# Kernel tuning notes

Measured on AMD Instinct MI355X. Metric: run time of the kernel, lower is better.

Reference implementation:

```python
import jax, jax.numpy as jnp
import numpy as np

B, T, C, H, L, V = 8, 512, 512, 8, 2, 512
DH = C // H
SCALE = 1.0 / np.sqrt(DH)


def _ln(x, g, b):
    mu = jnp.mean(x, -1, keepdims=True)
    var = jnp.mean((x - mu) ** 2, -1, keepdims=True)
    return (x - mu) * jax.lax.rsqrt(var + 1e-5) * g + b


def setup_inputs() -> dict:
    key = jax.random.key(0)
    ks = jax.random.split(key, 16)
    f = lambda k, shape: jax.random.normal(k, shape, jnp.float32) * 0.02
    return {
        "idx": jax.random.randint(ks[0], (B, T), 0, 4),
        "tok_emb": f(ks[1], (4, C)),
        "pos_emb": f(ks[2], (T, C)),
        "ln1_g": jnp.ones((L, C)), "ln1_b": jnp.zeros((L, C)),
        "Wq": f(ks[3], (L, C, C)), "bq": jnp.zeros((L, C)),
        "Wk": f(ks[4], (L, C, C)), "bk": jnp.zeros((L, C)),
        "Wv": f(ks[5], (L, C, C)), "bv": jnp.zeros((L, C)),
        "Wp": f(ks[6], (L, C, C)), "bp": jnp.zeros((L, C)),
        "ln2_g": jnp.ones((L, C)), "ln2_b": jnp.zeros((L, C)),
        "W1": f(ks[7], (L, C, 4 * C)), "b1": jnp.zeros((L, 4 * C)),
        "W2": f(ks[8], (L, 4 * C, C)), "b2": jnp.zeros((L, C)),
        "lnf_g": jnp.ones((C,)), "lnf_b": jnp.zeros((C,)),
        "Whead": f(ks[9], (C, V)),
        "steps": 4,
    }


def _block(x, p):
    (l1g, l1b, wq, bq, wk, bk, wv, bv, wp, bp,
     l2g, l2b, w1, b1, w2, b2) = p
    # attention (mask buffer is all ones in the original -> full attention)
    xn = _ln(x, l1g, l1b)
    q = (xn @ wq + bq).reshape(B, T, H, DH)
    k = (xn @ wk + bk).reshape(B, T, H, DH)
    v = (xn @ wv + bv).reshape(B, T, H, DH)
    att = jnp.einsum('bqhd,bkhd->bhqk', q, k) * SCALE
    att = jax.nn.softmax(att, axis=-1)
    y = jnp.einsum('bhqk,bkhd->bqhd', att, v).reshape(B, T, C)
    x = x + y @ wp + bp
    # MLP with exact (erf) GELU, matching torch nn.GELU default
    h = jax.nn.gelu(_ln(x, l2g, l2b) @ w1 + b1, approximate=False)
    return x + h @ w2 + b2


def reference(idx, tok_emb, pos_emb, ln1_g, ln1_b, Wq, bq, Wk, bk, Wv, bv,
              Wp, bp, ln2_g, ln2_b, W1, b1, W2, b2, lnf_g, lnf_b, Whead,
              steps):
    params = (ln1_g, ln1_b, Wq, bq, Wk, bk, Wv, bv, Wp, bp,
              ln2_g, ln2_b, W1, b1, W2, b2)
    x = tok_emb[idx] + pos_emb[None, :, :]

    def run_blocks(x):
        def step(x, p):
            return _block(x, p), None
        x, _ = jax.lax.scan(step, x, params)
        return x

    for _ in range(steps):  # recurrent application of the whole stack
        x = run_blocks(x)
    x = _ln(x, lnf_g, lnf_b)
    return x @ Whead  # logits [B, T, V]
```

## Files before the change

kernel.cpp:

```cpp
#include <hip/hip_runtime.h>
#include <hip/hip_bf16.h>
#include <math.h>

#define BB 8
#define TT 512
#define CC 512
#define HH 8
#define DH 64
#define LL 2
#define VV 512
#define NSTEPS 4
#define BT (BB*TT)
#define FF (4*CC)

typedef unsigned short u16;
typedef __bf16 bf16x8 __attribute__((ext_vector_type(8)));
typedef float f32x4 __attribute__((ext_vector_type(4)));
typedef u16 u16x8 __attribute__((ext_vector_type(8)));

static __device__ __forceinline__ u16 f2bf(float f) {
    unsigned int u = __float_as_uint(f);
    unsigned int r = (u + 0x7fffu + ((u >> 16) & 1u)) >> 16;
    return (u16)r;
}

static __device__ __forceinline__ void async16(const void* g, void* l) {
    __builtin_amdgcn_global_load_lds((__attribute__((address_space(1))) void*)g,
                                     (__attribute__((address_space(3))) void*)l, 16, 0, 0);
}

static __device__ __forceinline__ int swzp(int r) { return (r ^ (r >> 2)) & 7; }

__global__ __launch_bounds__(256)
void prologue_kernel(const float* __restrict__ Wq, const float* __restrict__ Wk,
                     const float* __restrict__ Wv, const float* __restrict__ Wp,
                     const float* __restrict__ W1, const float* __restrict__ W2,
                     const float* __restrict__ Wh,
                     const float* __restrict__ ln1g, const float* __restrict__ ln1b,
                     const float* __restrict__ ln2g, const float* __restrict__ ln2b,
                     const float* __restrict__ lnfg, const float* __restrict__ lnfb,
                     u16* w_qkvt, u16* w_pt, u16* w_1t, u16* w_2t, u16* w_ht,
                     const int* __restrict__ idx, const float* __restrict__ tok,
                     const float* __restrict__ pos, float* __restrict__ x,
                     u16* __restrict__ xb, float* __restrict__ ucb,
                     float2* __restrict__ sp) {
    int bid = blockIdx.x;
    const size_t wcc = (size_t)CC*CC, wcf = (size_t)CC*FF;
    if (bid >= 1630) {
        int bt = bid - 1630;
        int t  = threadIdx.x;
        int token = idx[bt];
        int posrow = bt & (TT - 1);
        float v0 = tok[token*CC + t]       + pos[posrow*CC + t];
        float v1 = tok[token*CC + t + 256] + pos[posrow*CC + t + 256];
        size_t base = (size_t)bt*CC;
        x[base + t] = v0;            x[base + t + 256] = v1;
        xb[base + t] = f2bf(v0);     xb[base + t + 256] = f2bf(v1);
        float s = v0 + v1, q = v0*v0 + v1*v1;
#pragma unroll
        for (int off = 1; off < 64; off <<= 1) { s += __shfl_xor(s, off); q += __shfl_xor(q, off); }
        __shared__ float rs[4], rq[4];
        int wid = t >> 6, lane = t & 63;
        if (lane == 0) { rs[wid] = s; rq[wid] = q; }
        __syncthreads();
        if (t == 0)      sp[(size_t)bt*8] = make_float2(rs[0]+rs[1]+rs[2]+rs[3],
                                                        rq[0]+rq[1]+rq[2]+rq[3]);
        else if (t < 8)  sp[(size_t)bt*8 + t] = make_float2(0.f, 0.f);
        return;
    }
    if (bid >= 1600) {
        int c = (bid - 1600)*256 + threadIdx.x;
        const float* Wsrc; const float* gv; const float* bv2; float* up; float* cp;
        int n, Nd;
        if (c < 3072) {
            int l = c / 1536, w = c % 1536, m = w / 512; n = w % 512; Nd = CC;
            Wsrc = (m == 0 ? Wq : (m == 1 ? Wk : Wv)) + l*wcc;
            gv = ln1g + l*CC; bv2 = ln1b + l*CC;
            up = ucb + c; cp = ucb + 3072 + c;
        } else if (c < 7168) {
            int d = c - 3072, l = d / 2048; n = d % 2048; Nd = FF;
            Wsrc = W1 + l*wcf; gv = ln2g + l*CC; bv2 = ln2b + l*CC;
            up = ucb + 6144 + d; cp = ucb + 10240 + d;
        } else {
            n = c - 7168; Nd = VV; Wsrc = Wh; gv = lnfg; bv2 = lnfb;
            up = ucb + 14336 + n; cp = ucb + 14848 + n;
        }
        float su = 0.f, sc = 0.f;
        for (int k = 0; k < CC; k++) {
            float w = Wsrc[(size_t)k*Nd + n];
            su += gv[k]*w; sc += bv2[k]*w;
        }
        *up = su; *cp = sc;
        return;
    }
    const float* src; u16* dst; const float* gv = nullptr; int K, N, i0, j0;
    if (bid < 1536) {
        int l = bid / 768, r = bid % 768;
        if (r < 256) {
            int m = r / 64, t = r % 64;
            K = CC; N = CC;
            i0 = (t / 8) * 64; j0 = (t % 8) * 64;
            if      (m == 0) { src = Wq + l*wcc; dst = w_qkvt + (size_t)l*3*wcc;          gv = ln1g + l*CC; }
            else if (m == 1) { src = Wk + l*wcc; dst = w_qkvt + (size_t)l*3*wcc + wcc;    gv = ln1g + l*CC; }
            else if (m == 2) { src = Wv + l*wcc; dst = w_qkvt + (size_t)l*3*wcc + 2*wcc;  gv = ln1g + l*CC; }
            else             { src = Wp + l*wcc; dst = w_pt + (size_t)l*wcc; }
        } else if (r < 512) {
            int t = r - 256;
            K = CC; N = FF;
            i0 = (t / 32) * 64; j0 = (t % 32) * 64;
            src = W1 + l*wcf; dst = w_1t + (size_t)l*wcf; gv = ln2g + l*CC;
        } else {
            int t = r - 512;
            K = FF; N = CC;
            i0 = (t / 8) * 64; j0 = (t % 8) * 64;
            src = W2 + l*wcf; dst = w_2t + (size_t)l*wcf;
        }
    } else {
        int t = bid - 1536;
        K = CC; N = CC;
        i0 = (t / 8) * 64; j0 = (t % 8) * 64;
        src = Wh; dst = w_ht; gv = lnfg;
    }
    __shared__ float tile[64][65];
    int tt = threadIdx.x;
    int rr = tt >> 2, cg = (tt & 3) * 16;
    float gk = gv ? gv[i0 + rr] : 1.0f;
#pragma unroll
    for (int i = 0; i < 16; i++)
        tile[rr][cg + i] = src[(size_t)(i0 + rr) * N + j0 + cg + i] * gk;
    __syncthreads();
#pragma unroll
    for (int i = 0; i < 16; i++)
        dst[(size_t)(j0 + rr) * K + i0 + cg + i] = f2bf(tile[cg + i][rr]);
}

template<int BM, int BN, int THREADS, int WROWS, int WCOLS, int EPI>
__global__ __launch_bounds__(THREADS, 6)
void gemm_bt_kernel(const u16* __restrict__ A, const u16* __restrict__ Bt,
                    int N, int K,
                    const float* __restrict__ bias, const float* __restrict__ biask,
                    const float* __restrict__ biasv,
                    const float* __restrict__ uvec, const float* __restrict__ cvec,
                    const float2* __restrict__ spin, float2* __restrict__ spout,
                    float* outf, u16* outq, u16* outk, u16* outvt) {
    constexpr int WTM = BM / WROWS, WTN = BN / WCOLS;
    constexpr int TM = WTM / 16, TN = WTN / 16;
    constexpr bool FOLD = (EPI == 0 || EPI == 2 || EPI == 3);
    static_assert(THREADS == WROWS * WCOLS * 64, "wave grid");
    static_assert((8*BM) % THREADS == 0 && (8*BN) % THREADS == 0, "staging divisibility");
    static_assert(EPI != 1 || (BM == 32 && BN == 64 && WROWS == 2 && WCOLS == 2), "stats layout");
    __shared__ u16 lds_a[2][2][BM][32];
    __shared__ u16 lds_b[2][2][BN][32];
    __shared__ float s_rs[FOLD ? BM : 1], s_mrs[FOLD ? BM : 1];
    __shared__ float psum[EPI == 1 ? 2 : 1][BM], psq[EPI == 1 ? 2 : 1][BM];
    int tid = threadIdx.x;
    int wid = tid >> 6, lane = tid & 63;
    int quad = lane >> 4, l15 = lane & 15;
    int wm = (wid % WROWS) * WTM, wn = (wid / WROWS) * WTN;

    int NBN = N / BN;
    int lin = blockIdx.x;
    int x8 = lin & 7, slot = lin >> 3;
    int bn = slot % NBN;
    int bm = (slot / NBN) * 8 + x8;

    const size_t a0 = (size_t)bm * BM, b0 = (size_t)bn * BN;

    auto stage = [&](int buf, int kt) {
#pragma unroll
        for (int i = 0; i < (8*BM)/THREADS; i++) {
            int f = tid + i*THREADS;
            int ks2 = f / (4*BM), rem = f % (4*BM);
            int row = rem >> 2, c2 = rem & 3;
            int g = (ks2*4 + c2) ^ swzp(row);
            async16(&A[(a0 + row)*K + kt + g*8], (u16*)lds_a[buf] + (size_t)f*8);
        }
#pragma unroll
        for (int i = 0; i < (8*BN)/THREADS; i++) {
            int f = tid + i*THREADS;
            int ks2 = f / (4*BN), rem = f % (4*BN);
            int row = rem >> 2, c2 = rem & 3;
            int g = (ks2*4 + c2) ^ swzp(row);
            async16(&Bt[(b0 + row)*K + kt + g*8], (u16*)lds_b[buf] + (size_t)f*8);
        }
    };

    f32x4 zero = {0.f, 0.f, 0.f, 0.f};
    f32x4 acc[TM][TN];
#pragma unroll
    for (int mi = 0; mi < TM; mi++)
#pragma unroll
        for (int ni = 0; ni < TN; ni++) acc[mi][ni] = zero;

    stage(0, 0);
    __syncthreads();
    const int NKT = K / 64;
    for (int kt = 0; kt < NKT; kt++) {
        int cur = kt & 1;
        if (kt + 1 < NKT) stage(cur ^ 1, (kt + 1) * 64);
#pragma unroll
        for (int ks = 0; ks < 2; ks++) {
            bf16x8 af[TM], bfr[TN];
#pragma unroll
            for (int mi = 0; mi < TM; mi++) {
                int row = wm + mi*16 + l15;
                int lc = (ks*4 + quad) ^ swzp(row);
                af[mi] = *(const bf16x8*)&lds_a[cur][lc >> 2][row][(lc & 3) * 8];
            }
#pragma unroll
            for (int ni = 0; ni < TN; ni++) {
                int row = wn + ni*16 + l15;
                int lc = (ks*4 + quad) ^ swzp(row);
                bfr[ni] = *(const bf16x8*)&lds_b[cur][lc >> 2][row][(lc & 3) * 8];
            }
#pragma unroll
            for (int mi = 0; mi < TM; mi++)
#pragma unroll
                for (int ni = 0; ni < TN; ni++)
                    acc[mi][ni] = __builtin_amdgcn_mfma_f32_16x16x32_bf16(af[mi], bfr[ni], acc[mi][ni], 0, 0, 0);
        }
        __syncthreads();
    }

    if (FOLD) {
        for (int r = tid; r < BM; r += THREADS) {
            float s = 0.f, q = 0.f;
#pragma unroll
            for (int j = 0; j < 8; j++) { float2 p = spin[(a0 + r)*8 + j]; s += p.x; q += p.y; }
            float mu  = s * (1.0f / CC);
            float var = q * (1.0f / CC) - mu * mu;
            float rstd = rsqrtf(var + 1e-5f);
            s_rs[r] = rstd; s_mrs[r] = mu * rstd;
        }
        __syncthreads();
    }

    float lsum[TM][4], lsq[TM][4];
    if (EPI == 1) {
#pragma unroll
        for (int mi = 0; mi < TM; mi++)
#pragma unroll
            for (int i = 0; i < 4; i++) { lsum[mi][i] = 0.f; lsq[mi][i] = 0.f; }
    }

#pragma unroll
    for (int mi = 0; mi < TM; mi++)
#pragma unroll
        for (int ni = 0; ni < TN; ni++) {
            int col = bn*BN + wn + ni*16 + l15;
            float uc_ = 0.f, cc_ = 0.f;
            if (FOLD) { uc_ = uvec[col]; cc_ = cvec[col]; }
#pragma unroll
            for (int i = 0; i < 4; i++) {
                int rloc = wm + mi*16 + quad*4 + i;
                int row = bm*BM + rloc;
                float v = acc[mi][ni][i];
                if (FOLD) v = s_rs[rloc]*v - s_mrs[rloc]*uc_ + cc_;
                if (EPI == 0) {
                    int region = col >> 9, cl = col & 511;
                    if (region == 0) {
                        v = (v + bias[cl]) * 0.125f;
                        outq[(size_t)row*512 + cl] = f2bf(v);
                    } else if (region == 1) {
                        v += biask[cl];
                        outk[(size_t)row*512 + cl] = f2bf(v);
                    } else {
                        v += biasv[cl];
                        int bb = row >> 9, tpos = row & 511, hh = cl >> 6, dh = cl & 63;
                        outvt[(((size_t)(bb*8 + hh)*64 + dh) << 9) + tpos] = f2bf(v);
                    }
                } else if (EPI == 1) {
                    size_t id2 = (size_t)row * N + col;
                    v += bias[col] + outf[id2];
                    outf[id2] = v;
                    outq[id2] = f2bf(v);
                    lsum[mi][i] += v; lsq[mi][i] += v*v;
                } else if (EPI == 2) {
                    v += bias[col];
                    v = 0.5f * v * (1.0f + erff(v * 0.70710678118654752f));
                    outq[(size_t)row * N + col] = f2bf(v);
                } else {
                    outf[(size_t)row * N + col] = v;
                }
            }
        }

    if (EPI == 1) {
#pragma unroll
        for (int mi = 0; mi < TM; mi++)
#pragma unroll
            for (int i = 0; i < 4; i++) {
                float s = lsum[mi][i], q = lsq[mi][i];
#pragma unroll
                for (int off = 1; off < 16; off <<= 1) { s += __shfl_xor(s, off); q += __shfl_xor(q, off); }
                if (l15 == 0) {
                    int pr = wm + mi*16 + quad*4 + i;
                    psum[wn >> 5][pr] = s; psq[wn >> 5][pr] = q;
                }
            }
        __syncthreads();
        if (tid < BM) {
            spout[(a0 + tid)*8 + bn] = make_float2(psum[0][tid] + psum[1][tid],
                                                   psq[0][tid] + psq[1][tid]);
        }
    }
}

__global__ __launch_bounds__(256)
void attn_mfma_kernel(const u16* __restrict__ q, const u16* __restrict__ k,
                      const u16* __restrict__ vt, u16* __restrict__ y) {
    __shared__ u16 lq[64][64];
    __shared__ u16 lk[2][64][64];
    __shared__ u16 lv[2][64][64];
    __shared__ u16 lp[4][16][72];
    int qt = blockIdx.x, h = blockIdx.y, b = blockIdx.z;
    int tid = threadIdx.x;
    int wid = tid >> 6, lane = tid & 63;
    int quad = lane >> 4, l15 = lane & 15;
    const int sr = tid >> 3;
    const int sc = (tid & 7) * 8;
    const int gsc = (((tid & 7) ^ swzp(sr)) << 3);

    auto stageKV = [&](int buf, int kt) {
#pragma unroll
        for (int c = 0; c < 2; c++) {
            async16(&k[(size_t)(b*TT + kt*64 + c*32 + sr)*CC + h*DH + gsc], &lk[buf][c*32 + sr][sc]);
            async16(&vt[((size_t)((b*HH + h)*DH + c*32 + sr))*TT + kt*64 + gsc], &lv[buf][c*32 + sr][sc]);
        }
    };

#pragma unroll
    for (int c = 0; c < 2; c++)
        async16(&q[(size_t)(b*TT + qt*64 + c*32 + sr)*CC + h*DH + gsc], &lq[c*32 + sr][sc]);
    stageKV(0, 0);
    __syncthreads();

    f32x4 zero = {0.f, 0.f, 0.f, 0.f};
    f32x4 acc_o[4];
    float m_st[4], l_st[4];
#pragma unroll
    for (int i = 0; i < 4; i++) { m_st[i] = -INFINITY; l_st[i] = 0.f; }
#pragma unroll
    for (int ni = 0; ni < 4; ni++) acc_o[ni] = zero;

    const int rowq = wid*16 + l15;
    const int pq = swzp(rowq);

    for (int kt = 0; kt < TT/64; kt++) {
        int cur = kt & 1;
        if (kt + 1 < TT/64) stageKV(cur ^ 1, kt + 1);

        f32x4 s[4];
#pragma unroll
        for (int ni = 0; ni < 4; ni++) s[ni] = zero;
#pragma unroll
        for (int ks = 0; ks < 2; ks++) {
            int lcq = (ks*4 + quad) ^ pq;
            bf16x8 aq = *(const bf16x8*)&lq[rowq][lcq * 8];
            bf16x8 bfr[4];
#pragma unroll
            for (int ni = 0; ni < 4; ni++) {
                int rowk = ni*16 + l15;
                int lck = (ks*4 + quad) ^ swzp(rowk);
                bfr[ni] = *(const bf16x8*)&lk[cur][rowk][lck * 8];
            }
#pragma unroll
            for (int ni = 0; ni < 4; ni++)
                s[ni] = __builtin_amdgcn_mfma_f32_16x16x32_bf16(aq, bfr[ni], s[ni], 0, 0, 0);
        }

#pragma unroll
        for (int i = 0; i < 4; i++) {
            float mx = -INFINITY;
#pragma unroll
            for (int ni = 0; ni < 4; ni++) mx = fmaxf(mx, s[ni][i]);
#pragma unroll
            for (int off = 1; off < 16; off <<= 1) mx = fmaxf(mx, __shfl_xor(mx, off));
            float mn = fmaxf(m_st[i], mx);
            float al = __expf(m_st[i] - mn);
            float rs = 0.f;
#pragma unroll
            for (int ni = 0; ni < 4; ni++) {
                float p = __expf(s[ni][i] - mn);
                s[ni][i] = p;
                rs += p;
            }
#pragma unroll
            for (int off = 1; off < 16; off <<= 1) rs += __shfl_xor(rs, off);
            l_st[i] = l_st[i] * al + rs;
            m_st[i] = mn;
#pragma unroll
            for (int ni = 0; ni < 4; ni++) acc_o[ni][i] *= al;
        }

#pragma unroll
        for (int ni = 0; ni < 4; ni++)
#pragma unroll
            for (int i = 0; i < 4; i++)
                lp[wid][quad*4 + i][ni*16 + l15] = f2bf(s[ni][i]);

#pragma unroll
        for (int ks = 0; ks < 2; ks++) {
            bf16x8 pa = *(const bf16x8*)&lp[wid][l15][ks*32 + quad*8];
            bf16x8 vb[4];
#pragma unroll
            for (int ni = 0; ni < 4; ni++) {
                int rowv = ni*16 + l15;
                int lcv = (ks*4 + quad) ^ swzp(rowv);
                vb[ni] = *(const bf16x8*)&lv[cur][rowv][lcv * 8];
            }
#pragma unroll
            for (int ni = 0; ni < 4; ni++)
                acc_o[ni] = __builtin_amdgcn_mfma_f32_16x16x32_bf16(pa, vb[ni], acc_o[ni], 0, 0, 0);
        }
        __syncthreads();
    }

#pragma unroll
    for (int i = 0; i < 4; i++) {
        float inv = 1.0f / l_st[i];
#pragma unroll
        for (int ni = 0; ni < 4; ni++) {
            int qrow = qt*64 + wid*16 + quad*4 + i;
            int col  = h*DH + ni*16 + l15;
            y[(size_t)(b*TT + qrow)*CC + col] = f2bf(acc_o[ni][i] * inv);
        }
    }
}

extern "C" void kernel_launch(void* const* d_in, const int* in_sizes, int n_in,
                              void* d_out, int out_size, void* d_ws, size_t ws_size,
                              hipStream_t stream) {
    const int*   idx   = (const int*)d_in[0];
    const float* tok   = (const float*)d_in[1];
    const float* pos   = (const float*)d_in[2];
    const float* ln1g  = (const float*)d_in[3];
    const float* ln1b  = (const float*)d_in[4];
    const float* Wq    = (const float*)d_in[5];
    const float* bq    = (const float*)d_in[6];
    const float* Wk    = (const float*)d_in[7];
    const float* bk    = (const float*)d_in[8];
    const float* Wv    = (const float*)d_in[9];
    const float* bv    = (const float*)d_in[10];
    const float* Wp    = (const float*)d_in[11];
    const float* bp    = (const float*)d_in[12];
    const float* ln2g  = (const float*)d_in[13];
    const float* ln2b  = (const float*)d_in[14];
    const float* W1    = (const float*)d_in[15];
    const float* b1    = (const float*)d_in[16];
    const float* W2    = (const float*)d_in[17];
    const float* b2    = (const float*)d_in[18];
    const float* lnfg  = (const float*)d_in[19];
    const float* lnfb  = (const float*)d_in[20];
    const float* Whead = (const float*)d_in[21];

    float* x  = (float*)d_ws;
    u16* xb   = (u16*)(x + (size_t)BT*CC);
    u16* yb   = xb + (size_t)BT*CC;
    u16* R    = yb + (size_t)BT*CC;
    u16* qb   = R;
    u16* kb   = R + (size_t)BT*CC;
    u16* vtb  = R + (size_t)2*BT*CC;
    u16* hb   = R;
    u16* w_qkvt = R + (size_t)4*BT*CC;
    u16* w_pt   = w_qkvt + (size_t)2*3*CC*CC;
    u16* w_1t   = w_pt   + (size_t)2*CC*CC;
    u16* w_2t   = w_1t   + (size_t)2*CC*FF;
    u16* w_ht   = w_2t   + (size_t)2*FF*CC;
    float* ucb  = (float*)(w_ht + (size_t)CC*VV);
    float2* sp  = (float2*)(ucb + 15360);

    prologue_kernel<<<1630 + BT, 256, 0, stream>>>(Wq, Wk, Wv, Wp, W1, W2, Whead,
                                                   ln1g, ln1b, ln2g, ln2b, lnfg, lnfb,
                                                   w_qkvt, w_pt, w_1t, w_2t, w_ht,
                                                   idx, tok, pos, x, xb, ucb, sp);

    const int g_qkv  = (3*CC/128) * (BT/64);
    const int g_fc1  = (FF/128)   * (BT/64);
    const int g_pf   = (CC/64)    * (BT/32);
    const int g_head = (VV/64)    * (BT/32);

    for (int s = 0; s < NSTEPS; s++) {
        for (int l = 0; l < LL; l++) {
            gemm_bt_kernel<64,128,512,2,4,0><<<g_qkv, 512, 0, stream>>>(
                xb, w_qkvt + (size_t)l*3*CC*CC, 3*CC, CC,
                bq + l*CC, bk + l*CC, bv + l*CC,
                ucb + l*1536, ucb + 3072 + l*1536, sp, nullptr,
                nullptr, qb, kb, vtb);
            attn_mfma_kernel<<<dim3(TT/64, HH, BB), 256, 0, stream>>>(qb, kb, vtb, yb);
            gemm_bt_kernel<32,64,256,2,2,1><<<g_pf, 256, 0, stream>>>(
                yb, w_pt + (size_t)l*CC*CC, CC, CC,
                bp + l*CC, nullptr, nullptr,
                nullptr, nullptr, nullptr, sp,
                x, xb, nullptr, nullptr);
            gemm_bt_kernel<64,128,512,2,4,2><<<g_fc1, 512, 0, stream>>>(
                xb, w_1t + (size_t)l*CC*FF, FF, CC,
                b1 + (size_t)l*FF, nullptr, nullptr,
                ucb + 6144 + l*2048, ucb + 10240 + l*2048, sp, nullptr,
                nullptr, hb, nullptr, nullptr);
            gemm_bt_kernel<32,64,256,2,2,1><<<g_pf, 256, 0, stream>>>(
                hb, w_2t + (size_t)l*FF*CC, CC, FF,
                b2 + l*CC, nullptr, nullptr,
                nullptr, nullptr, nullptr, sp,
                x, xb, nullptr, nullptr);
        }
    }

    gemm_bt_kernel<32,64,256,2,2,3><<<g_head, 256, 0, stream>>>(
        xb, w_ht, VV, CC,
        nullptr, nullptr, nullptr,
        ucb + 14336, ucb + 14848, sp, nullptr,
        (float*)d_out, nullptr, nullptr, nullptr);
}
```

Baseline: 907.6 us.

## Split LN-fold reductions over K, vectorize prologue, transpose attention score MFMA

The prologue's per-column LayerNorm-fold dot products are split across 8 K-chunks written to partial buffers, which the GEMM epilogues sum at read time. This gives more parallel blocks in place of a serial 512-long loop. The embedding and weight-transpose paths now use vector loads and stores, and the embedding path handles two rows per block. The attention kernel swaps the QK^T MFMA operands so each lane holds one query row, cutting softmax shuffles to two steps and enabling vectorized P stores to LDS. The cost is 8 extra loads per column in every fold epilogue and a cross-lane shuffle to broadcast alpha and l.

```diff
diff --git a/kernel.cpp b/kernel.cpp
--- a/kernel.cpp
+++ b/kernel.cpp
@@ -17,6 +17,7 @@
 typedef __bf16 bf16x8 __attribute__((ext_vector_type(8)));
 typedef float f32x4 __attribute__((ext_vector_type(4)));
 typedef u16 u16x8 __attribute__((ext_vector_type(8)));
+typedef u16 u16x4 __attribute__((ext_vector_type(4)));
 
 static __device__ __forceinline__ u16 f2bf(float f) {
     unsigned int u = __float_as_uint(f);
@@ -46,51 +47,64 @@
                      float2* __restrict__ sp) {
     int bid = blockIdx.x;
     const size_t wcc = (size_t)CC*CC, wcf = (size_t)CC*FF;
-    if (bid >= 1630) {
-        int bt = bid - 1630;
+    if (bid >= 1840) {
+        int eb = bid - 1840;
         int t  = threadIdx.x;
-        int token = idx[bt];
-        int posrow = bt & (TT - 1);
-        float v0 = tok[token*CC + t]       + pos[posrow*CC + t];
-        float v1 = tok[token*CC + t + 256] + pos[posrow*CC + t + 256];
-        size_t base = (size_t)bt*CC;
-        x[base + t] = v0;            x[base + t + 256] = v1;
-        xb[base + t] = f2bf(v0);     xb[base + t + 256] = f2bf(v1);
-        float s = v0 + v1, q = v0*v0 + v1*v1;
+        int r  = t >> 7, c4 = t & 127;
+        int row = eb*2 + r;
+        int token = idx[row];
+        int posrow = row & (TT - 1);
+        f32x4 v = ((const f32x4*)(tok + (size_t)token*CC))[c4]
+                + ((const f32x4*)(pos + (size_t)posrow*CC))[c4];
+        size_t base = (size_t)row*CC;
+        ((f32x4*)(x + base))[c4] = v;
+        u16x4 o;
+#pragma unroll
+        for (int j = 0; j < 4; j++) o[j] = f2bf(v[j]);
+        *(u16x4*)&xb[base + c4*4] = o;
+        float s = v[0]+v[1]+v[2]+v[3];
+        float q = v[0]*v[0]+v[1]*v[1]+v[2]*v[2]+v[3]*v[3];
 #pragma unroll
         for (int off = 1; off < 64; off <<= 1) { s += __shfl_xor(s, off); q += __shfl_xor(q, off); }
         __shared__ float rs[4], rq[4];
         int wid = t >> 6, lane = t & 63;
         if (lane == 0) { rs[wid] = s; rq[wid] = q; }
         __syncthreads();
-        if (t == 0)      sp[(size_t)bt*8] = make_float2(rs[0]+rs[1]+rs[2]+rs[3],
-                                                        rq[0]+rq[1]+rq[2]+rq[3]);
-        else if (t < 8)  sp[(size_t)bt*8 + t] = make_float2(0.f, 0.f);
+        if (t < 16) {
+            int r2 = t >> 3, slot = t & 7;
+            float2 val = (slot == 0)
+                ? make_float2(rs[r2*2] + rs[r2*2+1], rq[r2*2] + rq[r2*2+1])
+                : make_float2(0.f, 0.f);
+            sp[(size_t)(eb*2 + r2)*8 + slot] = val;
+        }
         return;
     }
     if (bid >= 1600) {
-        int c = (bid - 1600)*256 + threadIdx.x;
-        const float* Wsrc; const float* gv; const float* bv2; float* up; float* cp;
+        int d  = bid - 1600;
+        int j  = d & 7;
+        int cb = d >> 3;
+        int c  = cb*256 + threadIdx.x;
+        const float* Wsrc; const float* gv; const float* bv2;
         int n, Nd;
         if (c < 3072) {
             int l = c / 1536, w = c % 1536, m = w / 512; n = w % 512; Nd = CC;
             Wsrc = (m == 0 ? Wq : (m == 1 ? Wk : Wv)) + l*wcc;
             gv = ln1g + l*CC; bv2 = ln1b + l*CC;
-            up = ucb + c; cp = ucb + 3072 + c;
         } else if (c < 7168) {
-            int d = c - 3072, l = d / 2048; n = d % 2048; Nd = FF;
+            int dd = c - 3072, l = dd / 2048; n = dd % 2048; Nd = FF;
             Wsrc = W1 + l*wcf; gv = ln2g + l*CC; bv2 = ln2b + l*CC;
-            up = ucb + 6144 + d; cp = ucb + 10240 + d;
         } else {
             n = c - 7168; Nd = VV; Wsrc = Wh; gv = lnfg; bv2 = lnfb;
-            up = ucb + 14336 + n; cp = ucb + 14848 + n;
         }
         float su = 0.f, sc = 0.f;
-        for (int k = 0; k < CC; k++) {
-            float w = Wsrc[(size_t)k*Nd + n];
-            su += gv[k]*w; sc += bv2[k]*w;
-        }
-        *up = su; *cp = sc;
+        int k0 = j*64;
+#pragma unroll 4
+        for (int kk = 0; kk < 64; kk++) {
+            float w = Wsrc[(size_t)(k0 + kk)*Nd + n];
+            su += gv[k0 + kk]*w; sc += bv2[k0 + kk]*w;
+        }
+        ucb[j*7680 + c]         = su;
+        ucb[61440 + j*7680 + c] = sc;
         return;
     }
     const float* src; u16* dst; const float* gv = nullptr; int K, N, i0, j0;
@@ -122,16 +136,29 @@
         src = Wh; dst = w_ht; gv = lnfg;
     }
     __shared__ float tile[64][65];
+    __shared__ float gl[64];
     int tt = threadIdx.x;
     int rr = tt >> 2, cg = (tt & 3) * 16;
-    float gk = gv ? gv[i0 + rr] : 1.0f;
-#pragma unroll
-    for (int i = 0; i < 16; i++)
-        tile[rr][cg + i] = src[(size_t)(i0 + rr) * N + j0 + cg + i] * gk;
+    if (tt < 64) gl[tt] = gv ? gv[i0 + tt] : 1.0f;
+    {
+        const float* srow = &src[(size_t)(i0 + rr) * N + j0 + cg];
+        f32x4 v[4];
+#pragma unroll
+        for (int w = 0; w < 4; w++) v[w] = ((const f32x4*)srow)[w];
+#pragma unroll
+        for (int w = 0; w < 4; w++)
+#pragma unroll
+            for (int e = 0; e < 4; e++) tile[rr][cg + w*4 + e] = v[w][e];
+    }
     __syncthreads();
-#pragma unroll
-    for (int i = 0; i < 16; i++)
-        dst[(size_t)(j0 + rr) * K + i0 + cg + i] = f2bf(tile[cg + i][rr]);
+    u16x8 o0, o1;
+#pragma unroll
+    for (int i = 0; i < 8; i++) o0[i] = f2bf(tile[cg + i][rr]     * gl[cg + i]);
+#pragma unroll
+    for (int i = 0; i < 8; i++) o1[i] = f2bf(tile[cg + 8 + i][rr] * gl[cg + 8 + i]);
+    u16* drow = &dst[(size_t)(j0 + rr) * K + i0 + cg];
+    *(u16x8*)drow       = o0;
+    *(u16x8*)(drow + 8) = o1;
 }
 
 template<int BM, int BN, int THREADS, int WROWS, int WCOLS, int EPI>
@@ -249,7 +276,10 @@
         for (int ni = 0; ni < TN; ni++) {
             int col = bn*BN + wn + ni*16 + l15;
             float uc_ = 0.f, cc_ = 0.f;
-            if (FOLD) { uc_ = uvec[col]; cc_ = cvec[col]; }
+            if (FOLD) {
+#pragma unroll
+                for (int j = 0; j < 8; j++) { uc_ += uvec[j*7680 + col]; cc_ += cvec[j*7680 + col]; }
+            }
 #pragma unroll
             for (int i = 0; i < 4; i++) {
                 int rloc = wm + mi*16 + quad*4 + i;
@@ -337,9 +367,7 @@
 
     f32x4 zero = {0.f, 0.f, 0.f, 0.f};
     f32x4 acc_o[4];
-    float m_st[4], l_st[4];
-#pragma unroll
-    for (int i = 0; i < 4; i++) { m_st[i] = -INFINITY; l_st[i] = 0.f; }
+    float m_q = -INFINITY, l_q = 0.f;
 #pragma unroll
     for (int ni = 0; ni < 4; ni++) acc_o[ni] = zero;
 
@@ -366,38 +394,47 @@
             }
 #pragma unroll
             for (int ni = 0; ni < 4; ni++)
-                s[ni] = __builtin_amdgcn_mfma_f32_16x16x32_bf16(aq, bfr[ni], s[ni], 0, 0, 0);
-        }
-
-#pragma unroll
-        for (int i = 0; i < 4; i++) {
-            float mx = -INFINITY;
-#pragma unroll
-            for (int ni = 0; ni < 4; ni++) mx = fmaxf(mx, s[ni][i]);
-#pragma unroll
-            for (int off = 1; off < 16; off <<= 1) mx = fmaxf(mx, __shfl_xor(mx, off));
-            float mn = fmaxf(m_st[i], mx);
-            float al = __expf(m_st[i] - mn);
-            float rs = 0.f;
-#pragma unroll
-            for (int ni = 0; ni < 4; ni++) {
+                s[ni] = __builtin_amdgcn_mfma_f32_16x16x32_bf16(bfr[ni], aq, s[ni], 0, 0, 0);
+        }
+
+        float mx = s[0][0];
+#pragma unroll
+        for (int ni = 0; ni < 4; ni++)
+#pragma unroll
+            for (int i = 0; i < 4; i++) mx = fmaxf(mx, s[ni][i]);
+        mx = fmaxf(mx, __shfl_xor(mx, 16));
+        mx = fmaxf(mx, __shfl_xor(mx, 32));
+        float mn = fmaxf(m_q, mx);
+        float al = __expf(m_q - mn);
+        float rs = 0.f;
+#pragma unroll
+        for (int ni = 0; ni < 4; ni++)
+#pragma unroll
+            for (int i = 0; i < 4; i++) {
                 float p = __expf(s[ni][i] - mn);
                 s[ni][i] = p;
                 rs += p;
             }
-#pragma unroll
-            for (int off = 1; off < 16; off <<= 1) rs += __shfl_xor(rs, off);
-            l_st[i] = l_st[i] * al + rs;
-            m_st[i] = mn;
-#pragma unroll
-            for (int ni = 0; ni < 4; ni++) acc_o[ni][i] *= al;
-        }
-
+        rs += __shfl_xor(rs, 16);
+        rs += __shfl_xor(rs, 32);
+        l_q = l_q * al + rs;
+        m_q = mn;
+
+        float alb[4];
+#pragma unroll
+        for (int i = 0; i < 4; i++) alb[i] = __shfl(al, quad*4 + i);
 #pragma unroll
         for (int ni = 0; ni < 4; ni++)
 #pragma unroll
-            for (int i = 0; i < 4; i++)
-                lp[wid][quad*4 + i][ni*16 + l15] = f2bf(s[ni][i]);
+            for (int i = 0; i < 4; i++) acc_o[ni][i] *= alb[i];
+
+#pragma unroll
+        for (int ni = 0; ni < 4; ni++) {
+            u16x4 o;
+#pragma unroll
+            for (int i = 0; i < 4; i++) o[i] = f2bf(s[ni][i]);
+            *(u16x4*)&lp[wid][l15][ni*16 + quad*4] = o;
+        }
 
 #pragma unroll
         for (int ks = 0; ks < 2; ks++) {
@@ -416,9 +453,12 @@
         __syncthreads();
     }
 
+    float lb[4];
+#pragma unroll
+    for (int i = 0; i < 4; i++) lb[i] = __shfl(l_q, quad*4 + i);
 #pragma unroll
     for (int i = 0; i < 4; i++) {
-        float inv = 1.0f / l_st[i];
+        float inv = 1.0f / lb[i];
 #pragma unroll
         for (int ni = 0; ni < 4; ni++) {
             int qrow = qt*64 + wid*16 + quad*4 + i;
@@ -468,12 +508,12 @@
     u16* w_2t   = w_1t   + (size_t)2*CC*FF;
     u16* w_ht   = w_2t   + (size_t)2*FF*CC;
     float* ucb  = (float*)(w_ht + (size_t)CC*VV);
-    float2* sp  = (float2*)(ucb + 15360);
-
-    prologue_kernel<<<1630 + BT, 256, 0, stream>>>(Wq, Wk, Wv, Wp, W1, W2, Whead,
-                                                   ln1g, ln1b, ln2g, ln2b, lnfg, lnfb,
-                                                   w_qkvt, w_pt, w_1t, w_2t, w_ht,
-                                                   idx, tok, pos, x, xb, ucb, sp);
+    float2* sp  = (float2*)(ucb + 2*8*7680);
+
+    prologue_kernel<<<1840 + BT/2, 256, 0, stream>>>(Wq, Wk, Wv, Wp, W1, W2, Whead,
+                                                     ln1g, ln1b, ln2g, ln2b, lnfg, lnfb,
+                                                     w_qkvt, w_pt, w_1t, w_2t, w_ht,
+                                                     idx, tok, pos, x, xb, ucb, sp);
 
     const int g_qkv  = (3*CC/128) * (BT/64);
     const int g_fc1  = (FF/128)   * (BT/64);
@@ -485,7 +525,7 @@
             gemm_bt_kernel<64,128,512,2,4,0><<<g_qkv, 512, 0, stream>>>(
                 xb, w_qkvt + (size_t)l*3*CC*CC, 3*CC, CC,
                 bq + l*CC, bk + l*CC, bv + l*CC,
-                ucb + l*1536, ucb + 3072 + l*1536, sp, nullptr,
+                ucb + l*1536, ucb + 61440 + l*1536, sp, nullptr,
                 nullptr, qb, kb, vtb);
             attn_mfma_kernel<<<dim3(TT/64, HH, BB), 256, 0, stream>>>(qb, kb, vtb, yb);
             gemm_bt_kernel<32,64,256,2,2,1><<<g_pf, 256, 0, stream>>>(
@@ -496,7 +536,7 @@
             gemm_bt_kernel<64,128,512,2,4,2><<<g_fc1, 512, 0, stream>>>(
                 xb, w_1t + (size_t)l*CC*FF, FF, CC,
                 b1 + (size_t)l*FF, nullptr, nullptr,
-                ucb + 6144 + l*2048, ucb + 10240 + l*2048, sp, nullptr,
+                ucb + 3072 + l*2048, ucb + 61440 + 3072 + l*2048, sp, nullptr,
                 nullptr, hb, nullptr, nullptr);
             gemm_bt_kernel<32,64,256,2,2,1><<<g_pf, 256, 0, stream>>>(
                 hb, w_2t + (size_t)l*FF*CC, CC, FF,
@@ -509,6 +549,6 @@
     gemm_bt_kernel<32,64,256,2,2,3><<<g_head, 256, 0, stream>>>(
         xb, w_ht, VV, CC,
         nullptr, nullptr, nullptr,
-        ucb + 14336, ucb + 14848, sp, nullptr,
+        ucb + 7168, ucb + 61440 + 7168, sp, nullptr,
         (float*)d_out, nullptr, nullptr, nullptr);
 }
```

Result: faster. 860.5 us (-5.2%).
